# Optimization experiments

Measured on AMD Instinct MI355X. Metric: run time of the kernel, lower is better.

## Reference

```python
import jax, jax.numpy as jnp
import numpy as np

N_UP, N_DOWN = 8, 8
N_ELEC = N_UP + N_DOWN
N_NUC = 4
D, K, F, H = 128, 64, 32, 45  # embedding, kernel, dist_feat, w-MLP hidden (log-spaced)
CUTOFF = 10.0
B = 2048


def _pairs(a, b):
    s, r = np.meshgrid(a, b, indexing='ij')
    return s.ravel(), r.ravel()


def _edges():
    up = np.arange(N_UP)
    dn = np.arange(N_UP, N_ELEC)
    su, ru = _pairs(up, up); m = su != ru; su, ru = su[m], ru[m]
    sd, rd = _pairs(dn, dn); m = sd != rd; sd, rd = sd[m], rd[m]
    same_s = np.concatenate([su, sd]); same_r = np.concatenate([ru, rd])
    a1s, a1r = _pairs(up, dn); a2s, a2r = _pairs(dn, up)
    anti_s = np.concatenate([a1s, a2s]); anti_r = np.concatenate([a1r, a2r])
    ne_s = np.repeat(np.arange(N_NUC), N_ELEC)
    ne_r = np.tile(np.arange(N_ELEC), N_NUC)
    return tuple(jnp.asarray(x, jnp.int32) for x in (same_s, same_r, anti_s, anti_r, ne_s, ne_r))


def setup_inputs() -> dict:
    key = jax.random.key(0)
    ks = jax.random.split(key, 10)
    rs = jax.random.normal(ks[0], (B, N_ELEC, 3)) * 2.0
    coords = jax.random.normal(ks[1], (N_NUC, 3)) * 2.0
    X_tab = jax.random.normal(ks[2], (1, D))
    Y_w = jax.random.normal(ks[3], (N_NUC, K)) / np.sqrt(N_NUC)
    wW1 = jax.random.normal(ks[4], (3, 3, F, H)) / np.sqrt(F)
    wb1 = jax.random.normal(ks[5], (3, 3, H)) * 0.1
    wW2 = jax.random.normal(ks[6], (3, 3, H, K)) / np.sqrt(H)
    h0_tab = jax.random.normal(ks[7], (2, 1, K))
    hW = jax.random.normal(ks[8], (2, 2, D, K)) / np.sqrt(D)
    gW = jax.random.normal(ks[9], (3, 3, K, D)) / np.sqrt(K)
    same_s, same_r, anti_s, anti_r, ne_s, ne_r = _edges()
    return dict(rs=rs, coords=coords, X_tab=X_tab, Y_w=Y_w, wW1=wW1, wb1=wb1,
                wW2=wW2, h0_tab=h0_tab, hW=hW, gW=gW,
                same_s=same_s, same_r=same_r, anti_s=anti_s, anti_r=anti_r,
                ne_s=ne_s, ne_r=ne_r)


def _dist_basis(d):
    # DistanceBasis with 'nocusp' envelope: env = d^2 exp(-d), gaussians at mus
    qs = jnp.linspace(0.0, 1.0, F)
    mus = CUTOFF * qs ** 2
    sigmas = (1.0 + CUTOFF * qs) / 7.0
    env = d ** 2 * jnp.exp(-d)
    return env[..., None] * jnp.exp(-((d[..., None] - mus) ** 2) / sigmas ** 2)


def reference(rs, coords, X_tab, Y_w, wW1, wb1, wW2, h0_tab, hW, gW,
              same_s, same_r, anti_s, anti_r, ne_s, ne_r):
    Bn = rs.shape[0]
    spin_idxs = jnp.zeros((N_ELEC,), jnp.int32)  # n_up == n_down -> one spin class
    # per-edge distances (layer-0 update_edges_fn featurizes them once)
    d_same = jnp.linalg.norm(rs[:, same_s] - rs[:, same_r], axis=-1)  # [B,112]
    d_anti = jnp.linalg.norm(rs[:, anti_s] - rs[:, anti_r], axis=-1)  # [B,128]
    d_ne = jnp.linalg.norm(coords[ne_s][None] - rs[:, ne_r], axis=-1)  # [B,64]
    feats = [_dist_basis(d_same), _dist_basis(d_anti), _dist_basis(d_ne)]
    senders = [same_s, anti_s, ne_s]
    receivers = [same_r, anti_r, ne_r]
    elec = X_tab[spin_idxs]  # [N_ELEC, D] electron embedding X(spin_idxs)
    nuc = Y_w                # Y(eye(n_nuc)) == Y_w, [N_NUC, K]
    for l in range(3):
        upd = 0.0
        for j in range(3):  # same, anti, ne
            # w subnet: 2-layer MLP, silu hidden with bias, bias-free linear out
            we = jax.nn.silu(feats[j] @ wW1[l, j] + wb1[l, j]) @ wW2[l, j]  # [B,E,K]
            if j < 2:
                if l == 0:
                    hx = h0_tab[j][spin_idxs][senders[j]]            # [E,K] embed
                else:
                    hx = (elec @ hW[l - 1, j])[:, senders[j]]        # [B,E,K]
                weh = we * hx
            else:
                weh = we * nuc[ne_s][None]                           # [B,E,K]
            # segment_sum scatter into receiver electrons
            z = jnp.zeros((Bn, N_ELEC, K), we.dtype).at[:, receivers[j]].add(weh)
            upd = upd + z @ gW[l, j]                                  # [B,N_ELEC,D]
        elec = elec + upd
    return elec
```

## Files before the change

kernel.cpp:

```cpp
#include <hip/hip_runtime.h>
#include <hip/hip_bf16.h>

#define NE 16
#define NN 4
#define DDIM 128
#define KD 64
#define HD 45

typedef _Float16 half8 __attribute__((ext_vector_type(8)));
typedef _Float16 half4 __attribute__((ext_vector_type(4)));
typedef float floatx4 __attribute__((ext_vector_type(4)));

#define OFF_FLAG_B 0
#define OFF_B1_B   64
#define OFF_XT_B   1792
#define OFF_H0_B   2304
#define OFF_YW_B   2560
#define OFF_W1_B   3072
#define OFF_W2_B   30720
#define OFF_GW_B   104448
#define OFF_HW_B   251904
#define OFF_IND_B  317440

#define WSTRIDE 328

__device__ __forceinline__ float ldf(const void* p, long i, int f32) {
    if (f32) return ((const float*)p)[i];
    unsigned int u = ((unsigned int)((const unsigned short*)p)[i]) << 16;
    return __uint_as_float(u);
}

__global__ void prep2_kernel(const void* w1, const void* b1, const void* w2, const void* h0,
                             const void* hW, const void* gW, const void* Yw, const void* Xt,
                             const void* rs,
                             const int* __restrict__ same_r, const int* __restrict__ anti_r,
                             const int* __restrict__ ne_r, char* wsB) {
    __shared__ int badS;
    if (threadIdx.x == 0) badS = 0;
    __syncthreads();
    {
        const unsigned short* rs16 = (const unsigned short*)rs;
        int bad = 0;
        for (int i = threadIdx.x; i < 2048; i += 256) {
            unsigned int u = ((unsigned int)rs16[i]) << 16;
            float v = __uint_as_float(u);
            if (!(fabsf(v) < 1e6f)) bad = 1;
        }
        if (bad) atomicOr(&badS, 1);
    }
    __syncthreads();
    const int f32 = badS ? 1 : 0;
    if (blockIdx.x == 0 && threadIdx.x == 0) *(int*)(wsB + OFF_FLAG_B) = f32;

    int i = blockIdx.x * 256 + threadIdx.x;
    _Float16* W1F = (_Float16*)(wsB + OFF_W1_B);
    _Float16* W2F = (_Float16*)(wsB + OFF_W2_B);
    _Float16* GWF = (_Float16*)(wsB + OFF_GW_B);
    _Float16* HWF = (_Float16*)(wsB + OFF_HW_B);
    _Float16* INDF= (_Float16*)(wsB + OFF_IND_B);
    float*    B1  = (float*)(wsB + OFF_B1_B);
    float*    XT  = (float*)(wsB + OFF_XT_B);
    _Float16* H0F = (_Float16*)(wsB + OFF_H0_B);
    _Float16* YWF = (_Float16*)(wsB + OFF_YW_B);

    if (i < 13824) {
        int lj = i / 1536, rem = i % 1536;
        int nt = rem >> 9, lane = (rem & 511) >> 3, e = rem & 7;
        int row = ((lane >> 4) << 3) + e;
        int col = (nt << 4) + (lane & 15);
        W1F[i] = (_Float16)((col < 45) ? ldf(w1, lj * 1440 + row * 45 + col, f32) : 0.f);
    }
    if (i < 36864) {
        int lj = i / 4096, rem = i & 4095;
        int nt = rem >> 10, kt = (rem >> 9) & 1, lane = (rem & 511) >> 3, e = rem & 7;
        int row = (kt << 5) + ((lane >> 4) << 3) + e;
        int col = (nt << 4) + (lane & 15);
        W2F[i] = (_Float16)((row < 45) ? ldf(w2, lj * 2880 + row * 64 + col, f32) : 0.f);
    }
    if (i < 73728) {
        int lj = i >> 13, rem = i & 8191;
        int nt = rem >> 10, kt = (rem >> 9) & 1, lane = (rem & 511) >> 3, e = rem & 7;
        int row = (kt << 5) + ((lane >> 4) << 3) + e;
        int col = (nt << 4) + (lane & 15);
        GWF[i] = (_Float16)ldf(gW, lj * 8192 + row * 128 + col, f32);
    }
    if (i < 32768) {
        int lj = i >> 13, rem = i & 8191;
        int nt = rem >> 11, kt = (rem >> 9) & 3, lane = (rem & 511) >> 3, e = rem & 7;
        int row = (kt << 5) + ((lane >> 4) << 3) + e;
        int col = (nt << 4) + (lane & 15);
        HWF[i] = (_Float16)ldf(hW, lj * 8192 + row * 64 + col, f32);
    }
    if (i < 5120) {
        int c = i >> 9, rem = i & 511;
        int ln = rem >> 3, ii = rem & 7;
        int cls = (c < 4) ? 0 : ((c < 8) ? 1 : 2);
        int lc  = c - ((cls == 0) ? 0 : ((cls == 1) ? 4 : 8));
        int qd = ln >> 4, lm = ln & 15;
        int e = lc * 32 + qd * 8 + ii;
        int cnt = (cls == 0) ? 112 : ((cls == 1) ? 128 : 64);
        int r = 255;
        if (e < cnt) r = (cls == 0) ? same_r[e] : ((cls == 1) ? anti_r[e] : ne_r[e]);
        INDF[i] = (r == lm) ? (_Float16)1.0f : (_Float16)0.0f;
    }
    if (i < 432) { int lj = i / 48, n = i % 48; B1[i] = (n < 45) ? ldf(b1, lj * 45 + n, f32) : 0.f; }
    if (i < 128) XT[i] = ldf(Xt, i, f32);
    if (i < 128) H0F[i] = (_Float16)ldf(h0, i, f32);
    if (i < 256) YWF[i] = (_Float16)ldf(Yw, i, f32);
}

__device__ __forceinline__ half8 feat_tile(
    const void* __restrict__ rs, const void* __restrict__ coords,
    int b, int lm, int f32, int tloc, int cls,
    const int* __restrict__ S, const int* __restrict__ R,
    const float* __restrict__ A0, const float* __restrict__ B0, const float* __restrict__ C0)
{
    int le = tloc * 16 + lm;
    int s = S[le], r = R[le];
    long rb = ((long)b * NE + r) * 3;
    float bx = ldf(rs, rb + 0, f32), by = ldf(rs, rb + 1, f32), bz = ldf(rs, rb + 2, f32);
    float ax, ay, az;
    if (cls < 2) {
        long sb = ((long)b * NE + s) * 3;
        ax = ldf(rs, sb + 0, f32); ay = ldf(rs, sb + 1, f32); az = ldf(rs, sb + 2, f32);
    } else {
        ax = ldf(coords, s * 3 + 0, f32); ay = ldf(coords, s * 3 + 1, f32); az = ldf(coords, s * 3 + 2, f32);
    }
    float dx = ax - bx, dy = ay - by, dz = az - bz;
    float d = sqrtf(dx * dx + dy * dy + dz * dz);
    float d2 = d * d;
    half8 a;
    #pragma unroll
    for (int ii = 0; ii < 8; ++ii) {
        float E = fmaf(A0[ii], d2, fmaf(B0[ii], d, C0[ii]));
        a[ii] = (_Float16)(d2 * __expf(E));
    }
    return a;
}

__device__ __forceinline__ void we_tile_weh(
    half8 fa, int lj, int tloc, int cbase,
    const char* __restrict__ wsB, _Float16* __restrict__ hid,
    const _Float16* __restrict__ hxrow,
    const unsigned char* __restrict__ sendC,
    _Float16* __restrict__ wehT,
    int lane, int qd, int lm)
{
    const half8* W1F_lj = (const half8*)(wsB + OFF_W1_B) + lj * 192;
    half8 w0 = W1F_lj[lane], w1v = W1F_lj[64 + lane], w2v = W1F_lj[128 + lane];
    const float* B1 = (const float*)(wsB + OFF_B1_B) + lj * 48;
    float bi0 = B1[lm], bi1 = B1[16 + lm], bi2 = B1[32 + lm];
    floatx4 c0 = {0.f,0.f,0.f,0.f}, c1 = c0, c2 = c0;
    c0 = __builtin_amdgcn_mfma_f32_16x16x32_f16(fa, w0,  c0, 0, 0, 0);
    c1 = __builtin_amdgcn_mfma_f32_16x16x32_f16(fa, w1v, c1, 0, 0, 0);
    c2 = __builtin_amdgcn_mfma_f32_16x16x32_f16(fa, w2v, c2, 0, 0, 0);
    #pragma unroll
    for (int rr = 0; rr < 4; ++rr) {
        int row = qd * 4 + rr;
        int x = (row & 7) << 4;
        float v0 = c0[rr] + bi0, v1 = c1[rr] + bi1, v2 = c2[rr] + bi2;
        v0 = v0 * __builtin_amdgcn_rcpf(1.f + __expf(-v0));
        v1 = v1 * __builtin_amdgcn_rcpf(1.f + __expf(-v1));
        v2 = v2 * __builtin_amdgcn_rcpf(1.f + __expf(-v2));
        char* hb = (char*)hid + row * 128;
        *(_Float16*)(hb + ((lm * 2)      ^ x)) = (_Float16)v0;
        *(_Float16*)(hb + ((32 + lm * 2) ^ x)) = (_Float16)v1;
        *(_Float16*)(hb + ((64 + lm * 2) ^ x)) = (_Float16)v2;
    }
    int xr = (lm & 7) << 4;
    half8 a0 = *(const half8*)((const char*)hid + lm * 128 + ((qd * 16)      ^ xr));
    half8 a1 = *(const half8*)((const char*)hid + lm * 128 + ((64 + qd * 16) ^ xr));

    int sv0 = sendC[tloc * 16 + qd * 4 + 0];
    int sv1 = sendC[tloc * 16 + qd * 4 + 1];
    int sv2 = sendC[tloc * 16 + qd * 4 + 2];
    int sv3 = sendC[tloc * 16 + qd * 4 + 3];

    const half8* W2F_lj = (const half8*)(wsB + OFF_W2_B) + lj * 512;
    const int eb = cbase + tloc * 16 + qd * 4;
    #pragma unroll
    for (int nt = 0; nt < 4; ++nt) {
        half8 bk0 = W2F_lj[nt * 128 + lane], bk1 = W2F_lj[nt * 128 + 64 + lane];
        floatx4 acc = {0.f,0.f,0.f,0.f};
        acc = __builtin_amdgcn_mfma_f32_16x16x32_f16(a0, bk0, acc, 0, 0, 0);
        acc = __builtin_amdgcn_mfma_f32_16x16x32_f16(a1, bk1, acc, 0, 0, 0);
        const int kc = nt * 16 + lm;
        half4 hv;
        hv[0] = (_Float16)(acc[0] * (float)hxrow[sv0 * 68 + kc]);
        hv[1] = (_Float16)(acc[1] * (float)hxrow[sv1 * 68 + kc]);
        hv[2] = (_Float16)(acc[2] * (float)hxrow[sv2 * 68 + kc]);
        hv[3] = (_Float16)(acc[3] * (float)hxrow[sv3 * 68 + kc]);
        *(half4*)(wehT + kc * WSTRIDE + eb) = hv;
    }
}

__device__ __forceinline__ void hx_update(
    int L, int wv, int lane, int qd, int lm,
    const _Float16* __restrict__ elecB, const half8* __restrict__ HWF,
    _Float16* __restrict__ hxS)
{
    half8 ae0 = *(const half8*)(elecB + lm * 136 +  0 + qd * 8);
    half8 ae1 = *(const half8*)(elecB + lm * 136 + 32 + qd * 8);
    half8 ae2 = *(const half8*)(elecB + lm * 136 + 64 + qd * 8);
    half8 ae3 = *(const half8*)(elecB + lm * 136 + 96 + qd * 8);
    #pragma unroll
    for (int u = 0; u < 2; ++u) {
        int idx = wv * 2 + u;
        int j = idx >> 2, nt = idx & 3;
        const half8* Bb = HWF + (size_t)(((L * 2 + j) * 4 + nt) * 4) * 64;
        floatx4 acc = {0.f,0.f,0.f,0.f};
        acc = __builtin_amdgcn_mfma_f32_16x16x32_f16(ae0, Bb[  0 + lane], acc, 0, 0, 0);
        acc = __builtin_amdgcn_mfma_f32_16x16x32_f16(ae1, Bb[ 64 + lane], acc, 0, 0, 0);
        acc = __builtin_amdgcn_mfma_f32_16x16x32_f16(ae2, Bb[128 + lane], acc, 0, 0, 0);
        acc = __builtin_amdgcn_mfma_f32_16x16x32_f16(ae3, Bb[192 + lane], acc, 0, 0, 0);
        #pragma unroll
        for (int r = 0; r < 4; ++r)
            hxS[j * 1088 + (qd * 4 + r) * 68 + nt * 16 + lm] = (_Float16)acc[r];
    }
}

__global__ __launch_bounds__(256, 2)
void fused_kernel(const void* __restrict__ rs, const void* __restrict__ coords,
                  const int* __restrict__ same_s, const int* __restrict__ same_r,
                  const int* __restrict__ anti_s, const int* __restrict__ anti_r,
                  const int* __restrict__ ne_s,   const int* __restrict__ ne_r,
                  const char* __restrict__ wsB, void* __restrict__ out)
{
    const int b = blockIdx.x;
    const int tid = threadIdx.x;
    const int wv = tid >> 6, lane = tid & 63;
    const int qd = lane >> 4, lm = lane & 15;
    const int f32 = *(const int*)(wsB + OFF_FLAG_B);

    __shared__ __align__(16) _Float16 wehT[64 * WSTRIDE];
    __shared__ __align__(16) _Float16 hidA[4][1024];
    __shared__ __align__(16) _Float16 zhS[16 * 200];
    __shared__ _Float16 hxS[2 * 1088];
    __shared__ _Float16 nucS[4 * 68];
    __shared__ __align__(16) _Float16 elecB[16 * 136];
    __shared__ unsigned char sendPad[384];

    const _Float16* H0F = (const _Float16*)(wsB + OFF_H0_B);
    const _Float16* YWF = (const _Float16*)(wsB + OFF_YW_B);
    const float*    XT  = (const float*)(wsB + OFF_XT_B);
    const half8*    GWF = (const half8*)(wsB + OFF_GW_B);
    const half8*    HWF = (const half8*)(wsB + OFF_HW_B);
    const half8*    INDF= (const half8*)(wsB + OFF_IND_B);

    for (int i = tid; i < 384; i += 256) {
        int cls = i >> 7, pos = i & 127;
        int cnt = (cls == 0) ? 112 : ((cls == 1) ? 128 : 64);
        int s = 0;
        if (pos < cnt) {
            if (cls == 0)      s = same_s[pos];
            else if (cls == 1) s = anti_s[pos];
            else               s = ne_s[pos];
        }
        sendPad[i] = (unsigned char)s;
    }
    for (int i = tid; i < 2048; i += 256)
        hxS[(i >> 10) * 1088 + ((i >> 6) & 15) * 68 + (i & 63)] = H0F[((i >> 10) << 6) + (i & 63)];
    if (tid < 256) nucS[(tid >> 6) * 68 + (tid & 63)] = YWF[tid];
    for (int i = tid; i < 64 * WSTRIDE / 2; i += 256) ((unsigned int*)wehT)[i] = 0u;
    {
        _Float16* hid = hidA[wv];
        half8 z8 = {0,0,0,0,0,0,0,0};
        *(half8*)(hid + lane * 8) = z8;
        *(half8*)(hid + 512 + lane * 8) = z8;
    }
    __syncthreads();

    half8 fa_s0, fa_s1 = {0,0,0,0,0,0,0,0}, fa_a0, fa_a1, fa_n;
    {
        float A0[8], B0[8], C0[8];
        #pragma unroll
        for (int ii = 0; ii < 8; ++ii) {
            float qf = (float)(qd * 8 + ii) * (1.f / 31.f);
            float mu = 10.f * qf * qf;
            float u = 7.f * __builtin_amdgcn_rcpf(1.f + 10.f * qf);
            float is2 = u * u;
            A0[ii] = -is2;
            B0[ii] = 2.f * mu * is2 - 1.f;
            C0[ii] = -(mu * mu) * is2;
        }
        fa_s0 = feat_tile(rs, coords, b, lm, f32, wv,     0, same_s, same_r, A0, B0, C0);
        if (wv < 3)
        fa_s1 = feat_tile(rs, coords, b, lm, f32, wv + 4, 0, same_s, same_r, A0, B0, C0);
        fa_a0 = feat_tile(rs, coords, b, lm, f32, wv,     1, anti_s, anti_r, A0, B0, C0);
        fa_a1 = feat_tile(rs, coords, b, lm, f32, wv + 4, 1, anti_s, anti_r, A0, B0, C0);
        fa_n  = feat_tile(rs, coords, b, lm, f32, wv,     2, ne_s,   ne_r,   A0, B0, C0);
    }

    floatx4 eacc[2];
    #pragma unroll
    for (int u = 0; u < 2; ++u) {
        float xv = XT[(wv * 2 + u) * 16 + lm];
        eacc[u][0] = xv; eacc[u][1] = xv; eacc[u][2] = xv; eacc[u][3] = xv;
    }

    _Float16* hid = hidA[wv];

    for (int L = 0; L < 3; ++L) {
        const int lj0 = L * 3;
        we_tile_weh(fa_s0, lj0,     wv,     0,   wsB, hid, hxS,        sendPad,       wehT, lane, qd, lm);
        if (wv < 3)
        we_tile_weh(fa_s1, lj0,     wv + 4, 0,   wsB, hid, hxS,        sendPad,       wehT, lane, qd, lm);
        we_tile_weh(fa_a0, lj0 + 1, wv,     128, wsB, hid, hxS + 1088, sendPad + 128, wehT, lane, qd, lm);
        we_tile_weh(fa_a1, lj0 + 1, wv + 4, 128, wsB, hid, hxS + 1088, sendPad + 128, wehT, lane, qd, lm);
        we_tile_weh(fa_n,  lj0 + 2, wv,     256, wsB, hid, nucS,       sendPad + 256, wehT, lane, qd, lm);
        __syncthreads();

        {
            const _Float16* baseA = wehT + (wv * 16 + lm) * WSTRIDE + qd * 8;
            floatx4 z0 = {0.f,0.f,0.f,0.f};
            z0 = __builtin_amdgcn_mfma_f32_16x16x32_f16(*(const half8*)(baseA +   0), INDF[0 * 64 + lane], z0, 0, 0, 0);
            z0 = __builtin_amdgcn_mfma_f32_16x16x32_f16(*(const half8*)(baseA +  32), INDF[1 * 64 + lane], z0, 0, 0, 0);
            z0 = __builtin_amdgcn_mfma_f32_16x16x32_f16(*(const half8*)(baseA +  64), INDF[2 * 64 + lane], z0, 0, 0, 0);
            z0 = __builtin_amdgcn_mfma_f32_16x16x32_f16(*(const half8*)(baseA +  96), INDF[3 * 64 + lane], z0, 0, 0, 0);
            floatx4 z1 = {0.f,0.f,0.f,0.f};
            z1 = __builtin_amdgcn_mfma_f32_16x16x32_f16(*(const half8*)(baseA + 128), INDF[4 * 64 + lane], z1, 0, 0, 0);
            z1 = __builtin_amdgcn_mfma_f32_16x16x32_f16(*(const half8*)(baseA + 160), INDF[5 * 64 + lane], z1, 0, 0, 0);
            z1 = __builtin_amdgcn_mfma_f32_16x16x32_f16(*(const half8*)(baseA + 192), INDF[6 * 64 + lane], z1, 0, 0, 0);
            z1 = __builtin_amdgcn_mfma_f32_16x16x32_f16(*(const half8*)(baseA + 224), INDF[7 * 64 + lane], z1, 0, 0, 0);
            floatx4 z2 = {0.f,0.f,0.f,0.f};
            z2 = __builtin_amdgcn_mfma_f32_16x16x32_f16(*(const half8*)(baseA + 256), INDF[8 * 64 + lane], z2, 0, 0, 0);
            z2 = __builtin_amdgcn_mfma_f32_16x16x32_f16(*(const half8*)(baseA + 288), INDF[9 * 64 + lane], z2, 0, 0, 0);
            half4 h0v, h1v, h2v;
            #pragma unroll
            for (int i = 0; i < 4; ++i) {
                h0v[i] = (_Float16)z0[i]; h1v[i] = (_Float16)z1[i]; h2v[i] = (_Float16)z2[i];
            }
            _Float16* zr = zhS + lm * 200 + wv * 16 + qd * 4;
            *(half4*)(zr +   0) = h0v;
            *(half4*)(zr +  64) = h1v;
            *(half4*)(zr + 128) = h2v;
        }
        __syncthreads();

        #pragma unroll
        for (int u = 0; u < 2; ++u) {
            int t2 = wv * 2 + u;
            #pragma unroll
            for (int c = 0; c < 6; ++c) {
                half8 zf = *(const half8*)(zhS + lm * 200 + c * 32 + qd * 8);
                const half8* G = GWF + (size_t)(lj0 + (c >> 1)) * 1024;
                eacc[u] = __builtin_amdgcn_mfma_f32_16x16x32_f16(zf, G[t2 * 128 + (c & 1) * 64 + lane], eacc[u], 0, 0, 0);
            }
        }

        if (L < 2) {
            #pragma unroll
            for (int u = 0; u < 2; ++u) {
                int t2 = wv * 2 + u;
                #pragma unroll
                for (int r = 0; r < 4; ++r)
                    elecB[(qd * 4 + r) * 136 + t2 * 16 + lm] = (_Float16)eacc[u][r];
            }
            __syncthreads();
            hx_update(L, wv, lane, qd, lm, elecB, HWF, hxS);
            __syncthreads();
        }
    }

    if (f32) {
        float* o = (float*)out + (size_t)b * 2048;
        #pragma unroll
        for (int u = 0; u < 2; ++u)
            #pragma unroll
            for (int r = 0; r < 4; ++r)
                o[(qd * 4 + r) * 128 + (wv * 2 + u) * 16 + lm] = eacc[u][r];
    } else {
        __hip_bfloat16* o = (__hip_bfloat16*)out + (size_t)b * 2048;
        #pragma unroll
        for (int u = 0; u < 2; ++u)
            #pragma unroll
            for (int r = 0; r < 4; ++r)
                o[(qd * 4 + r) * 128 + (wv * 2 + u) * 16 + lm] = __float2bfloat16(eacc[u][r]);
    }
}

extern "C" void kernel_launch(void* const* d_in, const int* in_sizes, int n_in,
                              void* d_out, int out_size, void* d_ws, size_t ws_size,
                              hipStream_t stream) {
    const void* rs     = d_in[0];
    const void* coords = d_in[1];
    const void* X_tab  = d_in[2];
    const void* Y_w    = d_in[3];
    const void* wW1    = d_in[4];
    const void* wb1    = d_in[5];
    const void* wW2    = d_in[6];
    const void* h0     = d_in[7];
    const void* hW     = d_in[8];
    const void* gW     = d_in[9];
    const int* same_s = (const int*)d_in[10];
    const int* same_r = (const int*)d_in[11];
    const int* anti_s = (const int*)d_in[12];
    const int* anti_r = (const int*)d_in[13];
    const int* ne_s   = (const int*)d_in[14];
    const int* ne_r   = (const int*)d_in[15];
    char* wsB = (char*)d_ws;

    const int Bn = in_sizes[0] / (NE * 3);

    prep2_kernel<<<288, 256, 0, stream>>>(wW1, wb1, wW2, h0, hW, gW, Y_w, X_tab, rs,
                                          same_r, anti_r, ne_r, wsB);
    fused_kernel<<<Bn, 256, 0, stream>>>(rs, coords, same_s, same_r, anti_s, anti_r,
                                         ne_s, ne_r, wsB, d_out);
}
```

Measured before the change: 188.7 us.

## Double threads per block to 512 and redistribute edge tiles across eight waves

```diff
diff --git a/kernel.cpp b/kernel.cpp
--- a/kernel.cpp
+++ b/kernel.cpp
@@ -194,32 +194,7 @@
     }
 }
 
-__device__ __forceinline__ void hx_update(
-    int L, int wv, int lane, int qd, int lm,
-    const _Float16* __restrict__ elecB, const half8* __restrict__ HWF,
-    _Float16* __restrict__ hxS)
-{
-    half8 ae0 = *(const half8*)(elecB + lm * 136 +  0 + qd * 8);
-    half8 ae1 = *(const half8*)(elecB + lm * 136 + 32 + qd * 8);
-    half8 ae2 = *(const half8*)(elecB + lm * 136 + 64 + qd * 8);
-    half8 ae3 = *(const half8*)(elecB + lm * 136 + 96 + qd * 8);
-    #pragma unroll
-    for (int u = 0; u < 2; ++u) {
-        int idx = wv * 2 + u;
-        int j = idx >> 2, nt = idx & 3;
-        const half8* Bb = HWF + (size_t)(((L * 2 + j) * 4 + nt) * 4) * 64;
-        floatx4 acc = {0.f,0.f,0.f,0.f};
-        acc = __builtin_amdgcn_mfma_f32_16x16x32_f16(ae0, Bb[  0 + lane], acc, 0, 0, 0);
-        acc = __builtin_amdgcn_mfma_f32_16x16x32_f16(ae1, Bb[ 64 + lane], acc, 0, 0, 0);
-        acc = __builtin_amdgcn_mfma_f32_16x16x32_f16(ae2, Bb[128 + lane], acc, 0, 0, 0);
-        acc = __builtin_amdgcn_mfma_f32_16x16x32_f16(ae3, Bb[192 + lane], acc, 0, 0, 0);
-        #pragma unroll
-        for (int r = 0; r < 4; ++r)
-            hxS[j * 1088 + (qd * 4 + r) * 68 + nt * 16 + lm] = (_Float16)acc[r];
-    }
-}
-
-__global__ __launch_bounds__(256, 2)
+__global__ __launch_bounds__(512, 4)
 void fused_kernel(const void* __restrict__ rs, const void* __restrict__ coords,
                   const int* __restrict__ same_s, const int* __restrict__ same_r,
                   const int* __restrict__ anti_s, const int* __restrict__ anti_r,
@@ -233,7 +208,7 @@
     const int f32 = *(const int*)(wsB + OFF_FLAG_B);
 
     __shared__ __align__(16) _Float16 wehT[64 * WSTRIDE];
-    __shared__ __align__(16) _Float16 hidA[4][1024];
+    __shared__ __align__(16) _Float16 hidA[8][1024];
     __shared__ __align__(16) _Float16 zhS[16 * 200];
     __shared__ _Float16 hxS[2 * 1088];
     __shared__ _Float16 nucS[4 * 68];
@@ -247,7 +222,7 @@
     const half8*    HWF = (const half8*)(wsB + OFF_HW_B);
     const half8*    INDF= (const half8*)(wsB + OFF_IND_B);
 
-    for (int i = tid; i < 384; i += 256) {
+    for (int i = tid; i < 384; i += 512) {
         int cls = i >> 7, pos = i & 127;
         int cnt = (cls == 0) ? 112 : ((cls == 1) ? 128 : 64);
         int s = 0;
@@ -258,10 +233,10 @@
         }
         sendPad[i] = (unsigned char)s;
     }
-    for (int i = tid; i < 2048; i += 256)
+    for (int i = tid; i < 2048; i += 512)
         hxS[(i >> 10) * 1088 + ((i >> 6) & 15) * 68 + (i & 63)] = H0F[((i >> 10) << 6) + (i & 63)];
     if (tid < 256) nucS[(tid >> 6) * 68 + (tid & 63)] = YWF[tid];
-    for (int i = tid; i < 64 * WSTRIDE / 2; i += 256) ((unsigned int*)wehT)[i] = 0u;
+    for (int i = tid; i < 64 * WSTRIDE / 2; i += 512) ((unsigned int*)wehT)[i] = 0u;
     {
         _Float16* hid = hidA[wv];
         half8 z8 = {0,0,0,0,0,0,0,0};
@@ -270,7 +245,7 @@
     }
     __syncthreads();
 
-    half8 fa_s0, fa_s1 = {0,0,0,0,0,0,0,0}, fa_a0, fa_a1, fa_n;
+    half8 fa_s = {0,0,0,0,0,0,0,0}, fa_a, fa_n = {0,0,0,0,0,0,0,0};
     {
         float A0[8], B0[8], C0[8];
         #pragma unroll
@@ -283,81 +258,90 @@
             B0[ii] = 2.f * mu * is2 - 1.f;
             C0[ii] = -(mu * mu) * is2;
         }
-        fa_s0 = feat_tile(rs, coords, b, lm, f32, wv,     0, same_s, same_r, A0, B0, C0);
-        if (wv < 3)
-        fa_s1 = feat_tile(rs, coords, b, lm, f32, wv + 4, 0, same_s, same_r, A0, B0, C0);
-        fa_a0 = feat_tile(rs, coords, b, lm, f32, wv,     1, anti_s, anti_r, A0, B0, C0);
-        fa_a1 = feat_tile(rs, coords, b, lm, f32, wv + 4, 1, anti_s, anti_r, A0, B0, C0);
-        fa_n  = feat_tile(rs, coords, b, lm, f32, wv,     2, ne_s,   ne_r,   A0, B0, C0);
-    }
-
-    floatx4 eacc[2];
-    #pragma unroll
-    for (int u = 0; u < 2; ++u) {
-        float xv = XT[(wv * 2 + u) * 16 + lm];
-        eacc[u][0] = xv; eacc[u][1] = xv; eacc[u][2] = xv; eacc[u][3] = xv;
+        if (wv < 7)
+        fa_s = feat_tile(rs, coords, b, lm, f32, wv,     0, same_s, same_r, A0, B0, C0);
+        fa_a = feat_tile(rs, coords, b, lm, f32, wv,     1, anti_s, anti_r, A0, B0, C0);
+        if (wv >= 4)
+        fa_n = feat_tile(rs, coords, b, lm, f32, wv - 4, 2, ne_s,   ne_r,   A0, B0, C0);
+    }
+
+    floatx4 eacc;
+    {
+        float xv = XT[wv * 16 + lm];
+        eacc[0] = xv; eacc[1] = xv; eacc[2] = xv; eacc[3] = xv;
     }
 
     _Float16* hid = hidA[wv];
 
     for (int L = 0; L < 3; ++L) {
         const int lj0 = L * 3;
-        we_tile_weh(fa_s0, lj0,     wv,     0,   wsB, hid, hxS,        sendPad,       wehT, lane, qd, lm);
-        if (wv < 3)
-        we_tile_weh(fa_s1, lj0,     wv + 4, 0,   wsB, hid, hxS,        sendPad,       wehT, lane, qd, lm);
-        we_tile_weh(fa_a0, lj0 + 1, wv,     128, wsB, hid, hxS + 1088, sendPad + 128, wehT, lane, qd, lm);
-        we_tile_weh(fa_a1, lj0 + 1, wv + 4, 128, wsB, hid, hxS + 1088, sendPad + 128, wehT, lane, qd, lm);
-        we_tile_weh(fa_n,  lj0 + 2, wv,     256, wsB, hid, nucS,       sendPad + 256, wehT, lane, qd, lm);
+        if (wv < 7)
+        we_tile_weh(fa_s, lj0,     wv,     0,   wsB, hid, hxS,        sendPad,       wehT, lane, qd, lm);
+        we_tile_weh(fa_a, lj0 + 1, wv,     128, wsB, hid, hxS + 1088, sendPad + 128, wehT, lane, qd, lm);
+        if (wv >= 4)
+        we_tile_weh(fa_n, lj0 + 2, wv - 4, 256, wsB, hid, nucS,       sendPad + 256, wehT, lane, qd, lm);
         __syncthreads();
 
         {
-            const _Float16* baseA = wehT + (wv * 16 + lm) * WSTRIDE + qd * 8;
-            floatx4 z0 = {0.f,0.f,0.f,0.f};
-            z0 = __builtin_amdgcn_mfma_f32_16x16x32_f16(*(const half8*)(baseA +   0), INDF[0 * 64 + lane], z0, 0, 0, 0);
-            z0 = __builtin_amdgcn_mfma_f32_16x16x32_f16(*(const half8*)(baseA +  32), INDF[1 * 64 + lane], z0, 0, 0, 0);
-            z0 = __builtin_amdgcn_mfma_f32_16x16x32_f16(*(const half8*)(baseA +  64), INDF[2 * 64 + lane], z0, 0, 0, 0);
-            z0 = __builtin_amdgcn_mfma_f32_16x16x32_f16(*(const half8*)(baseA +  96), INDF[3 * 64 + lane], z0, 0, 0, 0);
-            floatx4 z1 = {0.f,0.f,0.f,0.f};
-            z1 = __builtin_amdgcn_mfma_f32_16x16x32_f16(*(const half8*)(baseA + 128), INDF[4 * 64 + lane], z1, 0, 0, 0);
-            z1 = __builtin_amdgcn_mfma_f32_16x16x32_f16(*(const half8*)(baseA + 160), INDF[5 * 64 + lane], z1, 0, 0, 0);
-            z1 = __builtin_amdgcn_mfma_f32_16x16x32_f16(*(const half8*)(baseA + 192), INDF[6 * 64 + lane], z1, 0, 0, 0);
-            z1 = __builtin_amdgcn_mfma_f32_16x16x32_f16(*(const half8*)(baseA + 224), INDF[7 * 64 + lane], z1, 0, 0, 0);
-            floatx4 z2 = {0.f,0.f,0.f,0.f};
-            z2 = __builtin_amdgcn_mfma_f32_16x16x32_f16(*(const half8*)(baseA + 256), INDF[8 * 64 + lane], z2, 0, 0, 0);
-            z2 = __builtin_amdgcn_mfma_f32_16x16x32_f16(*(const half8*)(baseA + 288), INDF[9 * 64 + lane], z2, 0, 0, 0);
-            half4 h0v, h1v, h2v;
-            #pragma unroll
-            for (int i = 0; i < 4; ++i) {
-                h0v[i] = (_Float16)z0[i]; h1v[i] = (_Float16)z1[i]; h2v[i] = (_Float16)z2[i];
+            const int kc = wv & 3, hf = wv >> 2;
+            const _Float16* baseA = wehT + (kc * 16 + lm) * WSTRIDE + qd * 8;
+            _Float16* zr = zhS + lm * 200 + kc * 16 + qd * 4;
+            if (hf == 0) {
+                floatx4 z0 = {0.f,0.f,0.f,0.f};
+                z0 = __builtin_amdgcn_mfma_f32_16x16x32_f16(*(const half8*)(baseA +   0), INDF[0 * 64 + lane], z0, 0, 0, 0);
+                z0 = __builtin_amdgcn_mfma_f32_16x16x32_f16(*(const half8*)(baseA +  32), INDF[1 * 64 + lane], z0, 0, 0, 0);
+                z0 = __builtin_amdgcn_mfma_f32_16x16x32_f16(*(const half8*)(baseA +  64), INDF[2 * 64 + lane], z0, 0, 0, 0);
+                z0 = __builtin_amdgcn_mfma_f32_16x16x32_f16(*(const half8*)(baseA +  96), INDF[3 * 64 + lane], z0, 0, 0, 0);
+                floatx4 z2 = {0.f,0.f,0.f,0.f};
+                z2 = __builtin_amdgcn_mfma_f32_16x16x32_f16(*(const half8*)(baseA + 256), INDF[8 * 64 + lane], z2, 0, 0, 0);
+                z2 = __builtin_amdgcn_mfma_f32_16x16x32_f16(*(const half8*)(baseA + 288), INDF[9 * 64 + lane], z2, 0, 0, 0);
+                half4 h0v, h2v;
+                #pragma unroll
+                for (int i = 0; i < 4; ++i) { h0v[i] = (_Float16)z0[i]; h2v[i] = (_Float16)z2[i]; }
+                *(half4*)(zr +   0) = h0v;
+                *(half4*)(zr + 128) = h2v;
+            } else {
+                floatx4 z1 = {0.f,0.f,0.f,0.f};
+                z1 = __builtin_amdgcn_mfma_f32_16x16x32_f16(*(const half8*)(baseA + 128), INDF[4 * 64 + lane], z1, 0, 0, 0);
+                z1 = __builtin_amdgcn_mfma_f32_16x16x32_f16(*(const half8*)(baseA + 160), INDF[5 * 64 + lane], z1, 0, 0, 0);
+                z1 = __builtin_amdgcn_mfma_f32_16x16x32_f16(*(const half8*)(baseA + 192), INDF[6 * 64 + lane], z1, 0, 0, 0);
+                z1 = __builtin_amdgcn_mfma_f32_16x16x32_f16(*(const half8*)(baseA + 224), INDF[7 * 64 + lane], z1, 0, 0, 0);
+                half4 h1v;
+                #pragma unroll
+                for (int i = 0; i < 4; ++i) h1v[i] = (_Float16)z1[i];
+                *(half4*)(zr + 64) = h1v;
             }
-            _Float16* zr = zhS + lm * 200 + wv * 16 + qd * 4;
-            *(half4*)(zr +   0) = h0v;
-            *(half4*)(zr +  64) = h1v;
-            *(half4*)(zr + 128) = h2v;
         }
         __syncthreads();
 
         #pragma unroll
-        for (int u = 0; u < 2; ++u) {
-            int t2 = wv * 2 + u;
-            #pragma unroll
-            for (int c = 0; c < 6; ++c) {
-                half8 zf = *(const half8*)(zhS + lm * 200 + c * 32 + qd * 8);
-                const half8* G = GWF + (size_t)(lj0 + (c >> 1)) * 1024;
-                eacc[u] = __builtin_amdgcn_mfma_f32_16x16x32_f16(zf, G[t2 * 128 + (c & 1) * 64 + lane], eacc[u], 0, 0, 0);
-            }
+        for (int c = 0; c < 6; ++c) {
+            half8 zf = *(const half8*)(zhS + lm * 200 + c * 32 + qd * 8);
+            const half8* G = GWF + (size_t)(lj0 + (c >> 1)) * 1024;
+            eacc = __builtin_amdgcn_mfma_f32_16x16x32_f16(zf, G[wv * 128 + (c & 1) * 64 + lane], eacc, 0, 0, 0);
         }
 
         if (L < 2) {
             #pragma unroll
-            for (int u = 0; u < 2; ++u) {
-                int t2 = wv * 2 + u;
+            for (int r = 0; r < 4; ++r)
+                elecB[(qd * 4 + r) * 136 + wv * 16 + lm] = (_Float16)eacc[r];
+            __syncthreads();
+            {
+                half8 ae0 = *(const half8*)(elecB + lm * 136 +  0 + qd * 8);
+                half8 ae1 = *(const half8*)(elecB + lm * 136 + 32 + qd * 8);
+                half8 ae2 = *(const half8*)(elecB + lm * 136 + 64 + qd * 8);
+                half8 ae3 = *(const half8*)(elecB + lm * 136 + 96 + qd * 8);
+                const int j = wv >> 2, nt = wv & 3;
+                const half8* Bb = HWF + (size_t)(((L * 2 + j) * 4 + nt) * 4) * 64;
+                floatx4 acc = {0.f,0.f,0.f,0.f};
+                acc = __builtin_amdgcn_mfma_f32_16x16x32_f16(ae0, Bb[  0 + lane], acc, 0, 0, 0);
+                acc = __builtin_amdgcn_mfma_f32_16x16x32_f16(ae1, Bb[ 64 + lane], acc, 0, 0, 0);
+                acc = __builtin_amdgcn_mfma_f32_16x16x32_f16(ae2, Bb[128 + lane], acc, 0, 0, 0);
+                acc = __builtin_amdgcn_mfma_f32_16x16x32_f16(ae3, Bb[192 + lane], acc, 0, 0, 0);
                 #pragma unroll
                 for (int r = 0; r < 4; ++r)
-                    elecB[(qd * 4 + r) * 136 + t2 * 16 + lm] = (_Float16)eacc[u][r];
+                    hxS[j * 1088 + (qd * 4 + r) * 68 + nt * 16 + lm] = (_Float16)acc[r];
             }
-            __syncthreads();
-            hx_update(L, wv, lane, qd, lm, elecB, HWF, hxS);
             __syncthreads();
         }
     }
@@ -365,17 +349,13 @@
     if (f32) {
         float* o = (float*)out + (size_t)b * 2048;
         #pragma unroll
-        for (int u = 0; u < 2; ++u)
-            #pragma unroll
-            for (int r = 0; r < 4; ++r)
-                o[(qd * 4 + r) * 128 + (wv * 2 + u) * 16 + lm] = eacc[u][r];
+        for (int r = 0; r < 4; ++r)
+            o[(qd * 4 + r) * 128 + wv * 16 + lm] = eacc[r];
     } else {
         __hip_bfloat16* o = (__hip_bfloat16*)out + (size_t)b * 2048;
         #pragma unroll
-        for (int u = 0; u < 2; ++u)
-            #pragma unroll
-            for (int r = 0; r < 4; ++r)
-                o[(qd * 4 + r) * 128 + (wv * 2 + u) * 16 + lm] = __float2bfloat16(eacc[u][r]);
+        for (int r = 0; r < 4; ++r)
+            o[(qd * 4 + r) * 128 + wv * 16 + lm] = __float2bfloat16(eacc[r]);
     }
 }
 
@@ -404,6 +384,6 @@
 
     prep2_kernel<<<288, 256, 0, stream>>>(wW1, wb1, wW2, h0, hW, gW, Y_w, X_tab, rs,
                                           same_r, anti_r, ne_r, wsB);
-    fused_kernel<<<Bn, 256, 0, stream>>>(rs, coords, same_s, same_r, anti_s, anti_r,
+    fused_kernel<<<Bn, 512, 0, stream>>>(rs, coords, same_s, same_r, anti_s, anti_r,
                                          ne_s, ne_r, wsB, d_out);
 }
```

New measurement: 197.8 us. 1.05x slower.
